# Kernel tuning notes

Measured on AMD Instinct MI355X. Metric: run time of the kernel, lower is better.

## Reference

```python
import jax, jax.numpy as jnp
import numpy as np

N = 50000      # nodes
E = 1_600_000  # edges per metapath graph
M = 3          # meta-path patterns
D = 128        # feature dim (in_size == out_size, GraphConv has no weight)
H = 128        # semantic-attention hidden size


def setup_inputs() -> dict:
    key = jax.random.key(0)
    k1, k2, k3, k4 = jax.random.split(key, 4)
    h = jax.random.normal(k1, (N, D), dtype=jnp.float32)
    # edges[m, 0] = src node ids, edges[m, 1] = dst node ids for metapath m
    edges = jax.random.randint(k2, (M, 2, E), 0, N, dtype=jnp.int32)
    W1 = jax.random.normal(k3, (D, H), dtype=jnp.float32) * 0.05
    b1 = jnp.zeros((H,), dtype=jnp.float32)
    W2 = jax.random.normal(k4, (H, 1), dtype=jnp.float32) * 0.05
    return {"h": h, "edges": edges, "W1": W1, "b1": b1, "W2": W2}


def _graph_conv_both(h, src, dst, n):
    """DGL GraphConv(norm='both', weight=None, bias=None):
    out = D_in^{-1/2} * A @ (D_out^{-1/2} * h), zero degrees clamped to 1."""
    ones = jnp.ones_like(src, dtype=h.dtype)
    out_deg = jax.ops.segment_sum(ones, src, num_segments=n)
    in_deg = jax.ops.segment_sum(ones, dst, num_segments=n)
    norm_src = jax.lax.rsqrt(jnp.maximum(out_deg, 1.0))
    norm_dst = jax.lax.rsqrt(jnp.maximum(in_deg, 1.0))
    msg = (h * norm_src[:, None])[src]                  # [E, D] gather
    agg = jax.ops.segment_sum(msg, dst, num_segments=n)  # [N, D] scatter-add
    return agg * norm_dst[:, None]


def reference(h, edges, W1, b1, W2):
    n = h.shape[0]
    m = edges.shape[0]
    # One normalized sparse aggregation per meta-path (fixed small M).
    z = jnp.stack(
        [_graph_conv_both(h, edges[i, 0], edges[i, 1], n) for i in range(m)],
        axis=1,
    )  # [N, M, D]
    # Semantic attention: project -> tanh -> score, mean over nodes, softmax over M.
    w = jnp.mean(jnp.tanh(z @ W1 + b1) @ W2, axis=0)  # [M, 1]
    beta = jax.nn.softmax(w, axis=0)                  # [M, 1]
    return jnp.sum(beta[None, :, :] * z, axis=1)      # [N, D]
```

## Files before the change

### kernel.cpp

```cpp
#include <hip/hip_runtime.h>
#include <cstdint>
#include <cstddef>

typedef unsigned int  uint;
typedef unsigned short ushort;
typedef short bf16x8 __attribute__((ext_vector_type(8)));
typedef float f32x4  __attribute__((ext_vector_type(4)));

#define N_NODES 50000
#define N_EDGES 1600000
#define N_META  3
#define DIM     128

#define BKT       256
#define NBKT      196
#define CSR_CAP   10240
#define OCH       128
#define EPC       (N_EDGES / OCH)
#define OWORDS    12500
#define PREP_A    (N_META * OCH)
#define W1C_B     4

#define AT_TILE   64
#define AT_NBLK   782

__device__ __forceinline__ uint bf16rne(float f) {
    const uint u = __float_as_uint(f);
    return (u + 0x7FFFu + ((u >> 16) & 1u)) >> 16;
}
__device__ __forceinline__ float bflo(uint p) { return __uint_as_float(p << 16); }
__device__ __forceinline__ float bfhi(uint p) { return __uint_as_float(p & 0xFFFF0000u); }
__device__ __forceinline__ float fast_tanh(float x) {
    const float e = __expf(2.0f * x);
    return 1.0f - 2.0f / (e + 1.0f);
}

__global__ __launch_bounds__(256) void prep_kernel(
        const int* __restrict__ edges, const float* __restrict__ W1,
        uint* __restrict__ bhout, uint* __restrict__ partials,
        ushort* __restrict__ W1T) {
    __shared__ __align__(16) uint sh[OWORDS];
    __shared__ uint bh[NBKT];
    const int blk = blockIdx.x;
    if (blk < PREP_A) {
        const int m = blk >> 7, c = blk & 127;
        uint4* sh4 = reinterpret_cast<uint4*>(sh);
        for (int j = threadIdx.x; j < OWORDS / 4; j += 256)
            sh4[j] = make_uint4(0u, 0u, 0u, 0u);
        for (int j = threadIdx.x; j < NBKT; j += 256) bh[j] = 0;
        __syncthreads();
        const int* src = edges + (size_t)(2 * m) * N_EDGES;
        const int* dst = edges + (size_t)(2 * m + 1) * N_EDGES;
        const int beg = c * EPC;
        for (int i = beg + 4 * threadIdx.x; i + 4 <= beg + EPC; i += 1024) {
            const uint4 s4 = *reinterpret_cast<const uint4*>(src + i);
            const uint4 d4 = *reinterpret_cast<const uint4*>(dst + i);
            atomicAdd(&sh[s4.x >> 2], 1u << (8 * (s4.x & 3)));
            atomicAdd(&sh[s4.y >> 2], 1u << (8 * (s4.y & 3)));
            atomicAdd(&sh[s4.z >> 2], 1u << (8 * (s4.z & 3)));
            atomicAdd(&sh[s4.w >> 2], 1u << (8 * (s4.w & 3)));
            atomicAdd(&bh[d4.x >> 8], 1u);
            atomicAdd(&bh[d4.y >> 8], 1u);
            atomicAdd(&bh[d4.z >> 8], 1u);
            atomicAdd(&bh[d4.w >> 8], 1u);
        }
        __syncthreads();
        uint4* outp4 = reinterpret_cast<uint4*>(
            partials + (size_t)(m * OCH + c) * OWORDS);
        for (int j = threadIdx.x; j < OWORDS / 4; j += 256) outp4[j] = sh4[j];
        uint* bo = bhout + (size_t)(m * OCH + c) * NBKT;
        for (int j = threadIdx.x; j < NBKT; j += 256) bo[j] = bh[j];
    } else {
        const int base = (blk - PREP_A) * (DIM * DIM / W1C_B);
        for (int o = base + threadIdx.x; o < base + DIM * DIM / W1C_B; o += 256) {
            const int j = o >> 7, k = o & 127;
            W1T[o] = (ushort)bf16rne(W1[k * DIM + j]);
        }
    }
}

__global__ __launch_bounds__(256) void scan_nsrc_kernel(
        const uint* __restrict__ bhout, int* __restrict__ bucket_off,
        int* __restrict__ chunk_base, int* __restrict__ row_off,
        const uint* __restrict__ partials, float* __restrict__ nsrc) {
    const int blk = blockIdx.x;
    if (blk < N_META) {
        __shared__ int sc[256];
        const int m = blk, t = threadIdx.x;
        int v = 0;
        if (t < NBKT)
            for (int c = 0; c < OCH; ++c)
                v += (int)bhout[(size_t)(m * OCH + c) * NBKT + t];
        sc[t] = v;
        __syncthreads();
        for (int off = 1; off < 256; off <<= 1) {
            const int tt = (t >= off) ? sc[t - off] : 0;
            __syncthreads();
            sc[t] += tt;
            __syncthreads();
        }
        const int excl = sc[t] - v;
        if (t < NBKT) {
            bucket_off[m * (NBKT + 1) + t] = excl;
            int run = excl;
            for (int c = 0; c < OCH; ++c) {
                chunk_base[(size_t)(m * OCH + c) * NBKT + t] = run;
                run += (int)bhout[(size_t)(m * OCH + c) * NBKT + t];
            }
        }
        if (t == 0) {
            bucket_off[m * (NBKT + 1) + NBKT] = N_EDGES;
            row_off[m * (N_NODES + 1) + N_NODES] = N_EDGES;
        }
    } else {
        const int i = (blk - N_META) * 256 + threadIdx.x;
        if (i < N_META * N_NODES) {
            const int m = i / N_NODES, node = i - m * N_NODES;
            const int q = node >> 2, s8 = 8 * (node & 3);
            int s = 0;
#pragma unroll 8
            for (int c = 0; c < OCH; ++c)
                s += (partials[(size_t)(m * OCH + c) * OWORDS + q] >> s8) & 0xFF;
            nsrc[i] = rsqrtf(fmaxf((float)s, 1.0f));
        }
    }
}

__global__ __launch_bounds__(256) void scale_kernel(
        const float* __restrict__ h, const float* __restrict__ nsrc,
        ushort* __restrict__ hbm) {
    const int i = blockIdx.x * 256 + threadIdx.x;
    const int node = i >> 5;
    const float4 v = reinterpret_cast<const float4*>(h)[i];
    uint2* o = reinterpret_cast<uint2*>(hbm);
#pragma unroll
    for (int m = 0; m < N_META; ++m) {
        const float n = nsrc[m * N_NODES + node];
        uint2 p;
        p.x = bf16rne(v.x * n) | (bf16rne(v.y * n) << 16);
        p.y = bf16rne(v.z * n) | (bf16rne(v.w * n) << 16);
        o[(size_t)m * (N_NODES * DIM / 4) + i] = p;
    }
}

__global__ __launch_bounds__(256) void bin_kernel(
        const int* __restrict__ edges, const int* __restrict__ chunk_base,
        uint* __restrict__ pairs) {
    const int m = blockIdx.y, c = blockIdx.x;
    __shared__ int cur[NBKT];
    const int* cb = chunk_base + (size_t)(m * OCH + c) * NBKT;
    for (int j = threadIdx.x; j < NBKT; j += 256) cur[j] = cb[j];
    __syncthreads();
    const int* src = edges + (size_t)(2 * m) * N_EDGES;
    const int* dst = edges + (size_t)(2 * m + 1) * N_EDGES;
    const int beg = c * EPC;
    uint* pm = pairs + (size_t)m * N_EDGES;
    for (int i = beg + 4 * threadIdx.x; i + 4 <= beg + EPC; i += 1024) {
        const uint4 s4 = *reinterpret_cast<const uint4*>(src + i);
        const uint4 d4 = *reinterpret_cast<const uint4*>(dst + i);
        int p0 = atomicAdd(&cur[d4.x >> 8], 1);
        pm[p0] = (d4.x << 16) | s4.x;
        int p1 = atomicAdd(&cur[d4.y >> 8], 1);
        pm[p1] = (d4.y << 16) | s4.y;
        int p2 = atomicAdd(&cur[d4.z >> 8], 1);
        pm[p2] = (d4.z << 16) | s4.z;
        int p3 = atomicAdd(&cur[d4.w >> 8], 1);
        pm[p3] = (d4.w << 16) | s4.w;
    }
}

__global__ __launch_bounds__(256) void csr_kernel(
        const uint* __restrict__ pairs, const int* __restrict__ bucket_off,
        int* __restrict__ row_off, ushort* __restrict__ csr) {
    const int b = blockIdx.x, m = blockIdx.y;
    const int node_base = b * BKT;
    const int nb = min(BKT, N_NODES - node_base);
    __shared__ uint stage[CSR_CAP];
    __shared__ int hist[BKT];
    __shared__ int sc[BKT];
    __shared__ int cur[BKT];
    hist[threadIdx.x] = 0;
    __syncthreads();
    const int beg = bucket_off[m * (NBKT + 1) + b];
    const int end = bucket_off[m * (NBKT + 1) + b + 1];
    const int cnt = end - beg;
    const uint* pm = pairs + (size_t)m * N_EDGES + beg;
    for (int i = threadIdx.x; i < cnt; i += 256) {
        const uint p = pm[i];
        if (i < CSR_CAP) stage[i] = p;
        atomicAdd(&hist[(int)(p >> 16) - node_base], 1);
    }
    __syncthreads();
    const int v = hist[threadIdx.x];
    sc[threadIdx.x] = v;
    __syncthreads();
    for (int off = 1; off < BKT; off <<= 1) {
        const int t = (threadIdx.x >= off) ? sc[threadIdx.x - off] : 0;
        __syncthreads();
        sc[threadIdx.x] += t;
        __syncthreads();
    }
    const int excl = sc[threadIdx.x] - v;
    cur[threadIdx.x] = beg + excl;
    if (threadIdx.x < nb)
        row_off[m * (N_NODES + 1) + node_base + threadIdx.x] = beg + excl;
    __syncthreads();
    ushort* cm = csr + (size_t)m * N_EDGES;
    for (int i = threadIdx.x; i < cnt; i += 256) {
        const uint p = (i < CSR_CAP) ? stage[i] : pm[i];
        const int dl = (int)(p >> 16) - node_base;
        const int pos = atomicAdd(&cur[dl], 1);
        cm[pos] = (ushort)(p & 0xFFFFu);
    }
}

__global__ __launch_bounds__(256) void gather_kernel(
        const ushort* __restrict__ hbm, const ushort* __restrict__ csr,
        const int* __restrict__ row_off, ushort* __restrict__ zb) {
    const int m    = blockIdx.y;
    const int wave = threadIdx.x >> 6;
    const int lane = threadIdx.x & 63;
    const int q    = lane >> 4;
    const int c16  = lane & 15;
    const int node = blockIdx.x * 4 + wave;
    const int* ro = row_off + m * (N_NODES + 1);
    const int beg = ro[node];
    const int end = ro[node + 1];
    const ushort* srcs = csr + (size_t)m * N_EDGES;
    const ushort* tab  = hbm + (size_t)m * N_NODES * DIM;
    float acc[8] = {};
    int j = beg;
    for (; j + 16 <= end; j += 16) {
        int s[4]; uint4 hv[4];
#pragma unroll
        for (int u = 0; u < 4; ++u) s[u] = srcs[j + 4 * u + q];
#pragma unroll
        for (int u = 0; u < 4; ++u)
            hv[u] = *reinterpret_cast<const uint4*>(tab + (size_t)s[u] * DIM + c16 * 8);
#pragma unroll
        for (int u = 0; u < 4; ++u) {
            acc[0] += bflo(hv[u].x); acc[1] += bfhi(hv[u].x);
            acc[2] += bflo(hv[u].y); acc[3] += bfhi(hv[u].y);
            acc[4] += bflo(hv[u].z); acc[5] += bfhi(hv[u].z);
            acc[6] += bflo(hv[u].w); acc[7] += bfhi(hv[u].w);
        }
    }
    for (; j + 4 <= end; j += 4) {
        const int s0 = srcs[j + q];
        const uint4 hv = *reinterpret_cast<const uint4*>(tab + (size_t)s0 * DIM + c16 * 8);
        acc[0] += bflo(hv.x); acc[1] += bfhi(hv.x);
        acc[2] += bflo(hv.y); acc[3] += bfhi(hv.y);
        acc[4] += bflo(hv.z); acc[5] += bfhi(hv.z);
        acc[6] += bflo(hv.w); acc[7] += bfhi(hv.w);
    }
    if (j + q < end) {
        const int s0 = srcs[j + q];
        const uint4 hv = *reinterpret_cast<const uint4*>(tab + (size_t)s0 * DIM + c16 * 8);
        acc[0] += bflo(hv.x); acc[1] += bfhi(hv.x);
        acc[2] += bflo(hv.y); acc[3] += bfhi(hv.y);
        acc[4] += bflo(hv.z); acc[5] += bfhi(hv.z);
        acc[6] += bflo(hv.w); acc[7] += bfhi(hv.w);
    }
#pragma unroll
    for (int k = 0; k < 8; ++k) {
        acc[k] += __shfl_xor(acc[k], 16);
        acc[k] += __shfl_xor(acc[k], 32);
    }
    if (lane < 16) {
        const float nd = rsqrtf(fmaxf((float)(end - beg), 1.0f));
        uint4 o;
        o.x = bf16rne(acc[0] * nd) | (bf16rne(acc[1] * nd) << 16);
        o.y = bf16rne(acc[2] * nd) | (bf16rne(acc[3] * nd) << 16);
        o.z = bf16rne(acc[4] * nd) | (bf16rne(acc[5] * nd) << 16);
        o.w = bf16rne(acc[6] * nd) | (bf16rne(acc[7] * nd) << 16);
        *reinterpret_cast<uint4*>(
            zb + ((size_t)m * N_NODES + node) * DIM + c16 * 8) = o;
    }
}

__global__ __launch_bounds__(256) void attn_kernel(
        const ushort* __restrict__ zb, const ushort* __restrict__ W1T,
        const float* __restrict__ b1, const float* __restrict__ W2,
        float* __restrict__ wacc) {
    const int m   = blockIdx.y;
    const int tid = threadIdx.x;
    const int wv  = tid >> 6;
    const int l   = tid & 63;
    __shared__ __align__(16) ushort w1s[DIM * DIM];
    __shared__ float red[4];

    {
        const uint4* g = reinterpret_cast<const uint4*>(W1T);
        for (int i = tid; i < DIM * DIM / 8; i += 256) {
            const int j = i >> 4;
            const int slot = i ^ (j & 7);
            *reinterpret_cast<uint4*>(
                reinterpret_cast<char*>(w1s) + slot * 16) = g[i];
        }
    }
    __syncthreads();

    const int node_base = blockIdx.x * AT_TILE + wv * 16;
    const int row = l & 15;
    const int q   = l >> 4;
    int nload = node_base + row;
    if (nload >= N_NODES) nload = N_NODES - 1;
    const ushort* zrow = zb + ((size_t)m * N_NODES + nload) * DIM + q * 8;

    bf16x8 a[4];
#pragma unroll
    for (int kk = 0; kk < 4; ++kk)
        a[kk] = *reinterpret_cast<const bf16x8*>(zrow + kk * 32);

    f32x4 acc[8];
#pragma unroll
    for (int ct = 0; ct < 8; ++ct) acc[ct] = (f32x4){0.f, 0.f, 0.f, 0.f};

#pragma unroll
    for (int kk = 0; kk < 4; ++kk) {
#pragma unroll
        for (int ct = 0; ct < 8; ++ct) {
            const int j = ct * 16 + row;
            const int slot = (j * 16 + kk * 4 + q) ^ (j & 7);
            const bf16x8 b = *reinterpret_cast<const bf16x8*>(
                reinterpret_cast<char*>(w1s) + slot * 16);
            acc[ct] = __builtin_amdgcn_mfma_f32_16x16x32_bf16(
                a[kk], b, acc[ct], 0, 0, 0);
        }
    }

    float local = 0.0f;
#pragma unroll
    for (int ct = 0; ct < 8; ++ct) {
        const int j = ct * 16 + row;
        const float b1j = b1[j];
        const float w2j = W2[j];
#pragma unroll
        for (int r = 0; r < 4; ++r) {
            const int nd = node_base + q * 4 + r;
            if (nd < N_NODES)
                local += fast_tanh(acc[ct][r] + b1j) * w2j;
        }
    }
    for (int off = 32; off > 0; off >>= 1)
        local += __shfl_xor(local, off);
    if (l == 0) red[wv] = local;
    __syncthreads();
    if (tid == 0)
        atomicAdd(&wacc[m], red[0] + red[1] + red[2] + red[3]);
}

__global__ __launch_bounds__(256) void final_kernel(
        const ushort* __restrict__ zb, const float* __restrict__ wacc,
        float* __restrict__ out) {
    const int g = blockIdx.x * 256 + threadIdx.x;
    const float invN = 1.0f / (float)N_NODES;
    const float w0 = wacc[0] * invN, w1 = wacc[1] * invN, w2 = wacc[2] * invN;
    const float mx = fmaxf(w0, fmaxf(w1, w2));
    const float e0 = expf(w0 - mx), e1 = expf(w1 - mx), e2 = expf(w2 - mx);
    const float inv = 1.0f / (e0 + e1 + e2);
    const float beta[3] = {e0 * inv, e1 * inv, e2 * inv};
    float a[8] = {};
#pragma unroll
    for (int m = 0; m < N_META; ++m) {
        const uint4 v = reinterpret_cast<const uint4*>(zb)[
            (size_t)m * (N_NODES * DIM / 8) + g];
        const float bm = beta[m];
        a[0] = fmaf(bflo(v.x), bm, a[0]); a[1] = fmaf(bfhi(v.x), bm, a[1]);
        a[2] = fmaf(bflo(v.y), bm, a[2]); a[3] = fmaf(bfhi(v.y), bm, a[3]);
        a[4] = fmaf(bflo(v.z), bm, a[4]); a[5] = fmaf(bfhi(v.z), bm, a[5]);
        a[6] = fmaf(bflo(v.w), bm, a[6]); a[7] = fmaf(bfhi(v.w), bm, a[7]);
    }
    float4 o0 = {a[0], a[1], a[2], a[3]};
    float4 o1 = {a[4], a[5], a[6], a[7]};
    reinterpret_cast<float4*>(out)[(size_t)g * 2 + 0] = o0;
    reinterpret_cast<float4*>(out)[(size_t)g * 2 + 1] = o1;
}

extern "C" void kernel_launch(void* const* d_in, const int* in_sizes, int n_in,
                              void* d_out, int out_size, void* d_ws, size_t ws_size,
                              hipStream_t stream) {
    const float* h    = (const float*)d_in[0];
    const int*  edges = (const int*)d_in[1];
    const float* W1   = (const float*)d_in[2];
    const float* b1   = (const float*)d_in[3];
    const float* W2   = (const float*)d_in[4];
    float* out = (float*)d_out;

    char* p = (char*)d_ws;
    ushort* zb      = (ushort*)p;
    uint*  pairs    = (uint*)p;
    uint*  partials = (uint*)(p + (size_t)N_META * N_EDGES * 4);
    p += (size_t)N_META * N_NODES * DIM * 2;
    ushort* hbm     = (ushort*)p; p += (size_t)N_META * N_NODES * DIM * 2;
    ushort* csr     = (ushort*)p; p += (size_t)N_META * N_EDGES * 2;
    int* row_off    = (int*)p;    p += ((size_t)N_META * (N_NODES + 1) + 1) * 4;
    float* nsrc     = (float*)p;  p += (size_t)N_META * N_NODES * 4;
    float* wacc     = (float*)p;  p += 16 * 4;
    uint* bhout     = (uint*)p;   p += (size_t)N_META * OCH * NBKT * 4;
    int* chunk_base = (int*)p;    p += (size_t)N_META * OCH * NBKT * 4;
    int* bucket_off = (int*)p;    p += (size_t)N_META * (NBKT + 1) * 4 + 4;
    ushort* W1T     = (ushort*)p; p += (size_t)DIM * DIM * 2;

    hipMemsetAsync(wacc, 0, 16 * 4, stream);

    prep_kernel<<<dim3(PREP_A + W1C_B), 256, 0, stream>>>(
        edges, W1, bhout, partials, W1T);
    scan_nsrc_kernel<<<dim3(N_META + (N_META * N_NODES + 255) / 256), 256, 0, stream>>>(
        bhout, bucket_off, chunk_base, row_off, partials, nsrc);
    scale_kernel<<<dim3(N_NODES * DIM / 4 / 256), 256, 0, stream>>>(h, nsrc, hbm);
    bin_kernel<<<dim3(OCH, N_META), 256, 0, stream>>>(edges, chunk_base, pairs);
    csr_kernel<<<dim3(NBKT, N_META), 256, 0, stream>>>(pairs, bucket_off, row_off, csr);
    gather_kernel<<<dim3(N_NODES / 4, N_META), 256, 0, stream>>>(
        hbm, csr, row_off, zb);
    attn_kernel<<<dim3(AT_NBLK, N_META), 256, 0, stream>>>(zb, W1T, b1, W2, wacc);
    final_kernel<<<dim3(N_NODES * DIM / 8 / 256), 256, 0, stream>>>(zb, wacc, out);
}
```

Before: 381.9 us.

## Fuse bin and scale kernels; compute bucket totals via atomics in prep

Bucket totals are now accumulated with global atomics in prep_kernel, so the scan block no longer loops over 128 chunk histograms serially. The per-chunk base offsets are computed inside the binning blocks themselves, which removes the chunk_base array. The binning and h-scaling kernels are merged into one launch, saving a launch and letting the two independent workloads overlap. In exchange each bin block does a prefix loop over up to 127 chunk counts, and a larger memset is needed to zero the counters.

```diff
diff --git a/kernel.cpp b/kernel.cpp
--- a/kernel.cpp
+++ b/kernel.cpp
@@ -20,6 +20,7 @@
 #define OWORDS    12500
 #define PREP_A    (N_META * OCH)
 #define W1C_B     4
+#define SCALE_B   6250
 
 #define AT_TILE   64
 #define AT_NBLK   782
@@ -37,8 +38,8 @@
 
 __global__ __launch_bounds__(256) void prep_kernel(
         const int* __restrict__ edges, const float* __restrict__ W1,
-        uint* __restrict__ bhout, uint* __restrict__ partials,
-        ushort* __restrict__ W1T) {
+        uint* __restrict__ bhout, int* __restrict__ bucket_cnt,
+        uint* __restrict__ partials, ushort* __restrict__ W1T) {
     __shared__ __align__(16) uint sh[OWORDS];
     __shared__ uint bh[NBKT];
     const int blk = blockIdx.x;
@@ -69,7 +70,11 @@
             partials + (size_t)(m * OCH + c) * OWORDS);
         for (int j = threadIdx.x; j < OWORDS / 4; j += 256) outp4[j] = sh4[j];
         uint* bo = bhout + (size_t)(m * OCH + c) * NBKT;
-        for (int j = threadIdx.x; j < NBKT; j += 256) bo[j] = bh[j];
+        for (int j = threadIdx.x; j < NBKT; j += 256) {
+            const uint v = bh[j];
+            bo[j] = v;
+            if (v) atomicAdd(&bucket_cnt[m * NBKT + j], (int)v);
+        }
     } else {
         const int base = (blk - PREP_A) * (DIM * DIM / W1C_B);
         for (int o = base + threadIdx.x; o < base + DIM * DIM / W1C_B; o += 256) {
@@ -80,17 +85,14 @@
 }
 
 __global__ __launch_bounds__(256) void scan_nsrc_kernel(
-        const uint* __restrict__ bhout, int* __restrict__ bucket_off,
-        int* __restrict__ chunk_base, int* __restrict__ row_off,
-        const uint* __restrict__ partials, float* __restrict__ nsrc) {
+        const int* __restrict__ bucket_cnt, int* __restrict__ bucket_off,
+        int* __restrict__ row_off, const uint* __restrict__ partials,
+        float* __restrict__ nsrc) {
     const int blk = blockIdx.x;
     if (blk < N_META) {
         __shared__ int sc[256];
         const int m = blk, t = threadIdx.x;
-        int v = 0;
-        if (t < NBKT)
-            for (int c = 0; c < OCH; ++c)
-                v += (int)bhout[(size_t)(m * OCH + c) * NBKT + t];
+        const int v = (t < NBKT) ? bucket_cnt[m * NBKT + t] : 0;
         sc[t] = v;
         __syncthreads();
         for (int off = 1; off < 256; off <<= 1) {
@@ -100,14 +102,7 @@
             __syncthreads();
         }
         const int excl = sc[t] - v;
-        if (t < NBKT) {
-            bucket_off[m * (NBKT + 1) + t] = excl;
-            int run = excl;
-            for (int c = 0; c < OCH; ++c) {
-                chunk_base[(size_t)(m * OCH + c) * NBKT + t] = run;
-                run += (int)bhout[(size_t)(m * OCH + c) * NBKT + t];
-            }
-        }
+        if (t < NBKT) bucket_off[m * (NBKT + 1) + t] = excl;
         if (t == 0) {
             bucket_off[m * (NBKT + 1) + NBKT] = N_EDGES;
             row_off[m * (N_NODES + 1) + N_NODES] = N_EDGES;
@@ -126,46 +121,51 @@
     }
 }
 
-__global__ __launch_bounds__(256) void scale_kernel(
-        const float* __restrict__ h, const float* __restrict__ nsrc,
+__global__ __launch_bounds__(256) void bin_scale_kernel(
+        const int* __restrict__ edges, const uint* __restrict__ bhout,
+        const int* __restrict__ bucket_off, const float* __restrict__ h,
+        const float* __restrict__ nsrc, uint* __restrict__ pairs,
         ushort* __restrict__ hbm) {
-    const int i = blockIdx.x * 256 + threadIdx.x;
-    const int node = i >> 5;
-    const float4 v = reinterpret_cast<const float4*>(h)[i];
-    uint2* o = reinterpret_cast<uint2*>(hbm);
-#pragma unroll
-    for (int m = 0; m < N_META; ++m) {
-        const float n = nsrc[m * N_NODES + node];
-        uint2 p;
-        p.x = bf16rne(v.x * n) | (bf16rne(v.y * n) << 16);
-        p.y = bf16rne(v.z * n) | (bf16rne(v.w * n) << 16);
-        o[(size_t)m * (N_NODES * DIM / 4) + i] = p;
-    }
-}
-
-__global__ __launch_bounds__(256) void bin_kernel(
-        const int* __restrict__ edges, const int* __restrict__ chunk_base,
-        uint* __restrict__ pairs) {
-    const int m = blockIdx.y, c = blockIdx.x;
-    __shared__ int cur[NBKT];
-    const int* cb = chunk_base + (size_t)(m * OCH + c) * NBKT;
-    for (int j = threadIdx.x; j < NBKT; j += 256) cur[j] = cb[j];
-    __syncthreads();
-    const int* src = edges + (size_t)(2 * m) * N_EDGES;
-    const int* dst = edges + (size_t)(2 * m + 1) * N_EDGES;
-    const int beg = c * EPC;
-    uint* pm = pairs + (size_t)m * N_EDGES;
-    for (int i = beg + 4 * threadIdx.x; i + 4 <= beg + EPC; i += 1024) {
-        const uint4 s4 = *reinterpret_cast<const uint4*>(src + i);
-        const uint4 d4 = *reinterpret_cast<const uint4*>(dst + i);
-        int p0 = atomicAdd(&cur[d4.x >> 8], 1);
-        pm[p0] = (d4.x << 16) | s4.x;
-        int p1 = atomicAdd(&cur[d4.y >> 8], 1);
-        pm[p1] = (d4.y << 16) | s4.y;
-        int p2 = atomicAdd(&cur[d4.z >> 8], 1);
-        pm[p2] = (d4.z << 16) | s4.z;
-        int p3 = atomicAdd(&cur[d4.w >> 8], 1);
-        pm[p3] = (d4.w << 16) | s4.w;
+    const int blk = blockIdx.x;
+    if (blk < PREP_A) {
+        const int m = blk >> 7, c = blk & 127;
+        __shared__ int cur[NBKT];
+        for (int j = threadIdx.x; j < NBKT; j += 256) {
+            int base = bucket_off[m * (NBKT + 1) + j];
+            for (int cc = 0; cc < c; ++cc)
+                base += (int)bhout[(size_t)(m * OCH + cc) * NBKT + j];
+            cur[j] = base;
+        }
+        __syncthreads();
+        const int* src = edges + (size_t)(2 * m) * N_EDGES;
+        const int* dst = edges + (size_t)(2 * m + 1) * N_EDGES;
+        const int beg = c * EPC;
+        uint* pm = pairs + (size_t)m * N_EDGES;
+        for (int i = beg + 4 * threadIdx.x; i + 4 <= beg + EPC; i += 1024) {
+            const uint4 s4 = *reinterpret_cast<const uint4*>(src + i);
+            const uint4 d4 = *reinterpret_cast<const uint4*>(dst + i);
+            int p0 = atomicAdd(&cur[d4.x >> 8], 1);
+            pm[p0] = (d4.x << 16) | s4.x;
+            int p1 = atomicAdd(&cur[d4.y >> 8], 1);
+            pm[p1] = (d4.y << 16) | s4.y;
+            int p2 = atomicAdd(&cur[d4.z >> 8], 1);
+            pm[p2] = (d4.z << 16) | s4.z;
+            int p3 = atomicAdd(&cur[d4.w >> 8], 1);
+            pm[p3] = (d4.w << 16) | s4.w;
+        }
+    } else {
+        const int i = (blk - PREP_A) * 256 + threadIdx.x;
+        const int node = i >> 5;
+        const float4 v = reinterpret_cast<const float4*>(h)[i];
+        uint2* o = reinterpret_cast<uint2*>(hbm);
+#pragma unroll
+        for (int m = 0; m < N_META; ++m) {
+            const float n = nsrc[m * N_NODES + node];
+            uint2 p;
+            p.x = bf16rne(v.x * n) | (bf16rne(v.y * n) << 16);
+            p.y = bf16rne(v.z * n) | (bf16rne(v.w * n) << 16);
+            o[(size_t)m * (N_NODES * DIM / 4) + i] = p;
+        }
     }
 }
 
@@ -397,19 +397,19 @@
     int* row_off    = (int*)p;    p += ((size_t)N_META * (N_NODES + 1) + 1) * 4;
     float* nsrc     = (float*)p;  p += (size_t)N_META * N_NODES * 4;
     float* wacc     = (float*)p;  p += 16 * 4;
+    int* bucket_cnt = (int*)p;    p += (size_t)N_META * NBKT * 4;
+    int* bucket_off = (int*)p;    p += (size_t)N_META * (NBKT + 1) * 4 + 4;
     uint* bhout     = (uint*)p;   p += (size_t)N_META * OCH * NBKT * 4;
-    int* chunk_base = (int*)p;    p += (size_t)N_META * OCH * NBKT * 4;
-    int* bucket_off = (int*)p;    p += (size_t)N_META * (NBKT + 1) * 4 + 4;
     ushort* W1T     = (ushort*)p; p += (size_t)DIM * DIM * 2;
 
-    hipMemsetAsync(wacc, 0, 16 * 4, stream);
+    hipMemsetAsync(wacc, 0, (16 + (size_t)N_META * NBKT) * 4, stream);
 
     prep_kernel<<<dim3(PREP_A + W1C_B), 256, 0, stream>>>(
-        edges, W1, bhout, partials, W1T);
+        edges, W1, bhout, bucket_cnt, partials, W1T);
     scan_nsrc_kernel<<<dim3(N_META + (N_META * N_NODES + 255) / 256), 256, 0, stream>>>(
-        bhout, bucket_off, chunk_base, row_off, partials, nsrc);
-    scale_kernel<<<dim3(N_NODES * DIM / 4 / 256), 256, 0, stream>>>(h, nsrc, hbm);
-    bin_kernel<<<dim3(OCH, N_META), 256, 0, stream>>>(edges, chunk_base, pairs);
+        bucket_cnt, bucket_off, row_off, partials, nsrc);
+    bin_scale_kernel<<<dim3(PREP_A + SCALE_B), 256, 0, stream>>>(
+        edges, bhout, bucket_off, h, nsrc, pairs, hbm);
     csr_kernel<<<dim3(NBKT, N_META), 256, 0, stream>>>(pairs, bucket_off, row_off, csr);
     gather_kernel<<<dim3(N_NODES / 4, N_META), 256, 0, stream>>>(
         hbm, csr, row_off, zb);
```

New measurement: 373.7 us, median of 2. 2.1% less time.
